# Kernel optimization log

Measured on AMD Instinct MI355X. Metric: run time of the kernel, lower is better.

The kernel has to match this reference:

```python
import jax, jax.numpy as jnp
import numpy as np

LSTM_DIMS = 1024
T = 4096
D = 1024  # per-direction input width; must equal LSTM_DIMS (see original w shape)
CELL_CLIP = 3.0   # tf.raw_ops.BlockLSTM default
FORGET_BIAS = 1.0  # tf.raw_ops.BlockLSTM default


def setup_inputs() -> dict:
    key = jax.random.key(0)
    k1, k2, k3 = jax.random.split(key, 3)
    res_for_1 = jax.random.normal(k1, (1, T, D), dtype=jnp.float32)
    res_back_1 = jax.random.normal(k2, (1, T, D), dtype=jnp.float32)
    # GlorotUniform for w: shape [D + 2*H, 4*H]
    fan_in, fan_out = D + 2 * LSTM_DIMS, 4 * LSTM_DIMS
    limit = np.sqrt(6.0 / (fan_in + fan_out)).astype(np.float32)
    w = jax.random.uniform(k3, (fan_in, fan_out), dtype=jnp.float32,
                           minval=-limit, maxval=limit)
    return {"res_for_1": res_for_1, "res_back_1": res_back_1, "w": w}


def _bilstm(res_for_1, res_back_1, w):
    H = w.shape[1] // 4
    x_dim = 2 * res_for_1.shape[-1]
    # concatenate_lstm: vec[i] = concat(for[i], back[T-1-i]) -> [T, 2D]
    vec_for = jnp.concatenate([res_for_1[0], res_back_1[0][::-1]], axis=-1)
    vec_back = vec_for[::-1]
    xs = jnp.stack([vec_for, vec_back])            # [2, T, 2D]
    w_x, w_h = w[:x_dim], w[x_dim:]                # [2D,4H], [H,4H]
    # precompute input projection as one big GEMM (bias is zeros)
    zx = jnp.einsum('dtf,fg->dtg', xs, w_x)        # [2, T, 4H]

    def step(carry, zx_t):
        c, h = carry
        z = zx_t + h @ w_h                         # [4H]
        zi, zc, zf, zo = jnp.split(z, 4)           # BlockLSTM icfo order
        i = jax.nn.sigmoid(zi)
        ci = jnp.tanh(zc)
        f = jax.nn.sigmoid(zf + FORGET_BIAS)
        cs = jnp.clip(f * c + i * ci, -CELL_CLIP, CELL_CLIP)
        o = jax.nn.sigmoid(zo)
        h = o * jnp.tanh(cs)
        return (cs, h), h

    init = (jnp.zeros((H,), zx.dtype), jnp.zeros((H,), zx.dtype))

    def run(zx_dir):
        _, hs = jax.lax.scan(step, init, zx_dir)
        return hs                                  # [T, H]

    hs = jax.vmap(run)(zx)                         # [2, T, H]
    return hs[0], hs[1]                            # res_for_2, res_back_2


def reference(res_for_1, res_back_1, w):
    return _bilstm(res_for_1, res_back_1, w)
```

## Files before the change

kernel.cpp:

```cpp
#include <hip/hip_runtime.h>

#define T_STEPS 4096
#define HDIM 1024

typedef __bf16 bf16x8 __attribute__((ext_vector_type(8)));
typedef float f32x4 __attribute__((ext_vector_type(4)));
typedef _Float16 half2_t __attribute__((ext_vector_type(2)));

__device__ __forceinline__ unsigned short f2bf(float x) {
  unsigned u = __builtin_bit_cast(unsigned, x);
  u += 0x7fffu + ((u >> 16) & 1u);
  return (unsigned short)(u >> 16);
}
__device__ __forceinline__ float bf2f(unsigned short b) {
  unsigned u = ((unsigned)b) << 16;
  return __builtin_bit_cast(float, u);
}

__global__ __launch_bounds__(256) void build_xs(
    const float* __restrict__ rf, const float* __restrict__ rb,
    unsigned short* __restrict__ xs) {
  int idx = blockIdx.x * 256 + threadIdx.x;
  int e = idx * 4;
  int f = e & 2047;
  int td = e >> 11;
  int t = td & 4095;
  int d = td >> 12;
  bool lower = f < 1024;
  int f2 = f & 1023;
  int trow;
  if (d == 0) trow = lower ? t : (4095 - t);
  else        trow = lower ? (4095 - t) : t;
  const float* src = (lower ? rf : rb) + trow * 1024 + f2;
  float4 v = *(const float4*)src;
  ushort4 o = make_ushort4(f2bf(v.x), f2bf(v.y), f2bf(v.z), f2bf(v.w));
  *(ushort4*)(xs + e) = o;
}

__global__ __launch_bounds__(256) void transpose_wx(
    const float* __restrict__ w, unsigned short* __restrict__ wxT) {
  __shared__ float tile[64][65];
  int bid = blockIdx.x;
  int bf_ = bid / 64;
  int bg = bid % 64;
  int f0 = bf_ * 64, g0 = bg * 64;
  int tid = threadIdx.x;
#pragma unroll
  for (int s = 0; s < 16; ++s) {
    int idx = s * 256 + tid;
    int fl = idx >> 6, gl = idx & 63;
    tile[fl][gl] = w[(size_t)(f0 + fl) * 4096 + g0 + gl];
  }
  __syncthreads();
#pragma unroll
  for (int s = 0; s < 16; ++s) {
    int idx = s * 256 + tid;
    int gl = idx >> 6, fl = idx & 63;
    wxT[(size_t)(g0 + gl) * 2048 + f0 + fl] = f2bf(tile[fl][gl]);
  }
}

__global__ __launch_bounds__(256) void gemm_zx(
    const unsigned short* __restrict__ xs, const unsigned short* __restrict__ wxT,
    unsigned short* __restrict__ zxo) {
  __shared__ uint4 lds[1024];
  char* ldsb = (char*)lds;
  int bid = blockIdx.x;
  int by = bid >> 5;
  int bx = bid & 31;
  int tid = threadIdx.x, lane = tid & 63, wid = tid >> 6;
  int wr = wid >> 1, wc = wid & 1;
  const int arow0 = by * 128, bcol0 = bx * 128;

  f32x4 acc[4][4] = {};

  for (int kt = 0; kt < 64; ++kt) {
    int k0 = kt * 32;
#pragma unroll
    for (int s = 0; s < 2; ++s) {
      int c = tid + 256 * s;
      int L = c * 16;
      int P = L ^ (((L >> 6) & 7) << 4);
      int row = c >> 2, ko = (c & 3) * 8;
      uint4 av = *(const uint4*)(xs  + (size_t)(arow0 + row) * 2048 + k0 + ko);
      uint4 bv = *(const uint4*)(wxT + (size_t)(bcol0 + row) * 2048 + k0 + ko);
      *(uint4*)(ldsb + P) = av;
      *(uint4*)(ldsb + 8192 + P) = bv;
    }
    __syncthreads();

    bf16x8 afr[4], bfr[4];
#pragma unroll
    for (int i = 0; i < 4; ++i) {
      int arow = wr * 64 + i * 16 + (lane & 15);
      int L = arow * 64 + (lane >> 4) * 16;
      int P = L ^ ((arow & 7) << 4);
      afr[i] = *(bf16x8*)(ldsb + P);
      int brow = wc * 64 + i * 16 + (lane & 15);
      int L2 = brow * 64 + (lane >> 4) * 16;
      int P2 = L2 ^ ((brow & 7) << 4);
      bfr[i] = *(bf16x8*)(ldsb + 8192 + P2);
    }
#pragma unroll
    for (int mi = 0; mi < 4; ++mi)
#pragma unroll
      for (int ni = 0; ni < 4; ++ni)
        acc[mi][ni] = __builtin_amdgcn_mfma_f32_16x16x32_bf16(
            afr[mi], bfr[ni], acc[mi][ni], 0, 0, 0);
    __syncthreads();
  }

#pragma unroll
  for (int mi = 0; mi < 4; ++mi)
#pragma unroll
    for (int ni = 0; ni < 4; ++ni)
#pragma unroll
      for (int r = 0; r < 4; ++r) {
        int rrow = arow0 + wr * 64 + mi * 16 + (lane >> 4) * 4 + r;
        int col  = bcol0 + wc * 64 + ni * 16 + (lane & 15);
        zxo[(size_t)rrow * 4096 + col] = f2bf(acc[mi][ni][r]);
      }
}

__global__ __launch_bounds__(256) void pack_whp(
    const float* __restrict__ w, unsigned* __restrict__ whp) {
  int idx = blockIdx.x * 256 + threadIdx.x;
  int gc = idx & 4095;
  int k2 = idx >> 12;
  float w0 = w[(size_t)(2048 + 2 * k2) * 4096 + gc];
  float w1 = w[(size_t)(2048 + 2 * k2 + 1) * 4096 + gc];
  unsigned short a = __builtin_bit_cast(unsigned short, (_Float16)w0);
  unsigned short b = __builtin_bit_cast(unsigned short, (_Float16)w1);
  whp[idx] = ((unsigned)b << 16) | (unsigned)a;
}

__global__ __launch_bounds__(256) void clear_hcom(uint4* __restrict__ p) {
  p[(size_t)blockIdx.x * 256 + threadIdx.x] = uint4{0, 0, 0, 0};
}

__device__ __forceinline__ float sigm(float x) {
  return 1.0f / (1.0f + __expf(-x));
}
__device__ __forceinline__ float tanh_fast(float x) {
  float e = __expf(-2.0f * x);
  return (1.0f - e) / (1.0f + e);
}

__global__ __launch_bounds__(1024, 4) void lstm_rec(
    const unsigned short* __restrict__ zx,
    const unsigned* __restrict__ whp,
    float* __restrict__ hout,
    unsigned* __restrict__ hcom) {
  __shared__ unsigned short hstg[16][64];
  __shared__ float part[2][16][64];

  int bid = blockIdx.x;
  int dir = bid >> 6;
  int bslot = bid & 63;
  int jbase = bslot << 4;
  int tid = threadIdx.x;
  int wave = tid >> 6;
  int lane = tid & 63;
  int jj = lane & 15, g = lane >> 4;
  int gcol = (g << 10) + jbase + jj;

  unsigned wpk[32];
  {
    const unsigned* wp = whp + (size_t)(wave * 32) * 4096 + gcol;
#pragma unroll
    for (int i = 0; i < 32; ++i) wpk[i] = wp[(size_t)i * 4096];
#pragma unroll
    for (int i = 0; i < 32; ++i)
      asm volatile("v_mov_b32 %0, %0" : "+v"(wpk[i]));
  }

  float c_reg = 0.0f;
  const unsigned short* zrow = zx + (size_t)dir * T_STEPS * 4096;
  float* hrow = hout + (size_t)dir * T_STEPS * HDIM;
  unsigned* hcd = hcom + (size_t)dir * T_STEPS * HDIM;
  const unsigned* hp_slice = hcd + wave * 64 + lane;

  for (int t = 0; t < T_STEPS; ++t) {
    float zxv = 0.0f;
    if (wave == 15) zxv = bf2f(zrow[(size_t)t * 4096 + gcol]);

    unsigned short hbits = 0;
    if (t > 0) {
      const unsigned* hp = hp_slice + (size_t)(t - 1) * HDIM;
      unsigned want = (unsigned)t << 16;
      unsigned v;
      do {
        v = __hip_atomic_load(hp, __ATOMIC_RELAXED, __HIP_MEMORY_SCOPE_AGENT);
      } while (v < want);
      hbits = (unsigned short)v;
    }
    hstg[wave][lane] = hbits;
    asm volatile("s_waitcnt lgkmcnt(0)" ::: "memory");

    const unsigned* h2 = (const unsigned*)(&hstg[wave][0]);
    float acc = 0.0f;
#pragma unroll
    for (int i = 0; i < 32; ++i) {
      half2_t hh = __builtin_bit_cast(half2_t, h2[i]);
      half2_t ww = __builtin_bit_cast(half2_t, wpk[i]);
      acc = __builtin_amdgcn_fdot2(ww, hh, acc, false);
    }
    if (wave == 15) acc += zxv;
    part[t & 1][wave][lane] = acc;
    __syncthreads();

    if (wave == 0) {
      float z = 0.f;
#pragma unroll
      for (int q = 0; q < 16; ++q) z += part[t & 1][q][lane];
      float gz = (g == 2) ? z + 1.0f : z;
      float nl = (g == 1) ? tanh_fast(z) : sigm(gz);
      float iv = __shfl(nl, jj, 64);
      float cv = __shfl(nl, 16 + jj, 64);
      float fv = __shfl(nl, 32 + jj, 64);
      float ov = __shfl(nl, 48 + jj, 64);
      if (lane < 16) {
        float cs = fmaf(fv, c_reg, iv * cv);
        cs = fminf(3.0f, fmaxf(-3.0f, cs));
        c_reg = cs;
        float h = ov * tanh_fast(cs);
        if (t + 1 < T_STEPS) {
          unsigned short hb = __builtin_bit_cast(unsigned short, (_Float16)h);
          unsigned pk = ((unsigned)(t + 1) << 16) | (unsigned)hb;
          __hip_atomic_store(&hcd[(size_t)t * HDIM + jbase + lane], pk,
                             __ATOMIC_RELAXED, __HIP_MEMORY_SCOPE_AGENT);
        }
        hrow[(size_t)t * HDIM + jbase + lane] = h;
      }
    }
  }
}

extern "C" void kernel_launch(void* const* d_in, const int* in_sizes, int n_in,
                              void* d_out, int out_size, void* d_ws, size_t ws_size,
                              hipStream_t stream) {
  const float* rf = (const float*)d_in[0];
  const float* rb = (const float*)d_in[1];
  const float* w  = (const float*)d_in[2];
  float* out = (float*)d_out;

  char* ws = (char*)d_ws;
  unsigned short* zx  = (unsigned short*)ws;
  unsigned short* xs  = (unsigned short*)(ws + (64u << 20));
  unsigned*      hcom = (unsigned*)(ws + (64u << 20));
  unsigned short* wxT = (unsigned short*)(ws + (96u << 20));
  unsigned*      whp  = (unsigned*)(ws + (96u << 20));

  build_xs<<<16384, 256, 0, stream>>>(rf, rb, xs);
  transpose_wx<<<2048, 256, 0, stream>>>(w, wxT);
  gemm_zx<<<2048, 256, 0, stream>>>(xs, wxT, zx);
  pack_whp<<<8192, 256, 0, stream>>>(w, whp);
  clear_hcom<<<8192, 256, 0, stream>>>((uint4*)hcom);
  lstm_rec<<<128, 1024, 0, stream>>>(zx, whp, out, hcom);
}
```

Measured before the change: 6.339 ms.

## Pipeline spin-wait loads in asm and defer fp32 output writes to unpack kernel

The single-load atomic spin on the previous step's h value becomes an inline-asm loop that keeps four uncached global loads in flight, cutting the latency of each poll. The per-step fp32 h store in the recurrent loop is dropped, and a separate unpack_out kernel converts the packed fp16 h values from the communication buffer into the output afterward. The output now carries fp16 precision, and the hand-written asm with vcc/exec branching is fragile.

```diff
diff --git a/kernel.cpp b/kernel.cpp
--- a/kernel.cpp
+++ b/kernel.cpp
@@ -149,7 +149,6 @@
 __global__ __launch_bounds__(1024, 4) void lstm_rec(
     const unsigned short* __restrict__ zx,
     const unsigned* __restrict__ whp,
-    float* __restrict__ hout,
     unsigned* __restrict__ hcom) {
   __shared__ unsigned short hstg[16][64];
   __shared__ float part[2][16][64];
@@ -176,7 +175,6 @@
 
   float c_reg = 0.0f;
   const unsigned short* zrow = zx + (size_t)dir * T_STEPS * 4096;
-  float* hrow = hout + (size_t)dir * T_STEPS * HDIM;
   unsigned* hcd = hcom + (size_t)dir * T_STEPS * HDIM;
   const unsigned* hp_slice = hcd + wave * 64 + lane;
 
@@ -186,13 +184,50 @@
 
     unsigned short hbits = 0;
     if (t > 0) {
-      const unsigned* hp = hp_slice + (size_t)(t - 1) * HDIM;
+      unsigned long long a = (unsigned long long)(hp_slice + (size_t)(t - 1) * HDIM);
       unsigned want = (unsigned)t << 16;
-      unsigned v;
-      do {
-        v = __hip_atomic_load(hp, __ATOMIC_RELAXED, __HIP_MEMORY_SCOPE_AGENT);
-      } while (v < want);
-      hbits = (unsigned short)v;
+      unsigned got, p0, p1, p2, p3;
+      asm volatile(
+        "v_mov_b32 %0, 0\n\t"
+        "global_load_dword %2, %6, off sc0 sc1\n\t"
+        "global_load_dword %3, %6, off sc0 sc1\n\t"
+        "global_load_dword %4, %6, off sc0 sc1\n\t"
+        "global_load_dword %5, %6, off sc0 sc1\n\t"
+        "1:\n\t"
+        "s_waitcnt vmcnt(3)\n\t"
+        "v_cmp_le_u32 vcc, %7, %2\n\t"
+        "v_cndmask_b32 %0, %0, %2, vcc\n\t"
+        "global_load_dword %2, %6, off sc0 sc1\n\t"
+        "v_cmp_le_u32 vcc, %7, %0\n\t"
+        "s_andn2_b64 vcc, exec, vcc\n\t"
+        "s_cbranch_scc0 2f\n\t"
+        "s_waitcnt vmcnt(3)\n\t"
+        "v_cmp_le_u32 vcc, %7, %3\n\t"
+        "v_cndmask_b32 %0, %0, %3, vcc\n\t"
+        "global_load_dword %3, %6, off sc0 sc1\n\t"
+        "v_cmp_le_u32 vcc, %7, %0\n\t"
+        "s_andn2_b64 vcc, exec, vcc\n\t"
+        "s_cbranch_scc0 2f\n\t"
+        "s_waitcnt vmcnt(3)\n\t"
+        "v_cmp_le_u32 vcc, %7, %4\n\t"
+        "v_cndmask_b32 %0, %0, %4, vcc\n\t"
+        "global_load_dword %4, %6, off sc0 sc1\n\t"
+        "v_cmp_le_u32 vcc, %7, %0\n\t"
+        "s_andn2_b64 vcc, exec, vcc\n\t"
+        "s_cbranch_scc0 2f\n\t"
+        "s_waitcnt vmcnt(3)\n\t"
+        "v_cmp_le_u32 vcc, %7, %5\n\t"
+        "v_cndmask_b32 %0, %0, %5, vcc\n\t"
+        "global_load_dword %5, %6, off sc0 sc1\n\t"
+        "v_cmp_le_u32 vcc, %7, %0\n\t"
+        "s_andn2_b64 vcc, exec, vcc\n\t"
+        "s_cbranch_scc1 1b\n\t"
+        "2:\n\t"
+        "s_waitcnt vmcnt(0)"
+        : "=&v"(got), "+v"(a), "=&v"(p0), "=&v"(p1), "=&v"(p2), "=&v"(p3)
+        : "v"(a), "v"(want)
+        : "vcc", "memory");
+      hbits = (unsigned short)got;
     }
     hstg[wave][lane] = hbits;
     asm volatile("s_waitcnt lgkmcnt(0)" ::: "memory");
@@ -224,16 +259,25 @@
         cs = fminf(3.0f, fmaxf(-3.0f, cs));
         c_reg = cs;
         float h = ov * tanh_fast(cs);
-        if (t + 1 < T_STEPS) {
-          unsigned short hb = __builtin_bit_cast(unsigned short, (_Float16)h);
-          unsigned pk = ((unsigned)(t + 1) << 16) | (unsigned)hb;
-          __hip_atomic_store(&hcd[(size_t)t * HDIM + jbase + lane], pk,
-                             __ATOMIC_RELAXED, __HIP_MEMORY_SCOPE_AGENT);
-        }
-        hrow[(size_t)t * HDIM + jbase + lane] = h;
+        unsigned short hb = __builtin_bit_cast(unsigned short, (_Float16)h);
+        unsigned pk = ((unsigned)(t + 1) << 16) | (unsigned)hb;
+        __hip_atomic_store(&hcd[(size_t)t * HDIM + jbase + lane], pk,
+                           __ATOMIC_RELAXED, __HIP_MEMORY_SCOPE_AGENT);
       }
     }
   }
+}
+
+__global__ __launch_bounds__(256) void unpack_out(
+    const unsigned* __restrict__ hcom, float* __restrict__ out) {
+  int i = blockIdx.x * 256 + threadIdx.x;
+  uint4 v = ((const uint4*)hcom)[i];
+  float4 o;
+  o.x = (float)__builtin_bit_cast(_Float16, (unsigned short)v.x);
+  o.y = (float)__builtin_bit_cast(_Float16, (unsigned short)v.y);
+  o.z = (float)__builtin_bit_cast(_Float16, (unsigned short)v.z);
+  o.w = (float)__builtin_bit_cast(_Float16, (unsigned short)v.w);
+  ((float4*)out)[i] = o;
 }
 
 extern "C" void kernel_launch(void* const* d_in, const int* in_sizes, int n_in,
@@ -256,5 +300,6 @@
   gemm_zx<<<2048, 256, 0, stream>>>(xs, wxT, zx);
   pack_whp<<<8192, 256, 0, stream>>>(w, whp);
   clear_hcom<<<8192, 256, 0, stream>>>((uint4*)hcom);
-  lstm_rec<<<128, 1024, 0, stream>>>(zx, whp, out, hcom);
-}
+  lstm_rec<<<128, 1024, 0, stream>>>(zx, whp, hcom);
+  unpack_out<<<8192, 256, 0, stream>>>(hcom, out);
+}
```

New measurement: 7.421 ms. +17.1%, slower.

## Drop fp32 output store from recurrence; unpack fp16 h buffer afterward

Applied to the files above, without the earlier changes.

The recurrent kernel no longer writes fp32 h to the output each step. It writes only the packed fp16 h with a step tag to the communication buffer, and a new kernel converts that buffer to fp32 output after the recurrence. The LDS read of h is widened to 128-bit loads, and the dot product is split across four accumulators to shorten the dependency chain. This takes a global store off the serial critical path, but the output now carries fp16 precision and costs an extra pass over memory.

```diff
diff --git a/kernel.cpp b/kernel.cpp
--- a/kernel.cpp
+++ b/kernel.cpp
@@ -149,7 +149,6 @@
 __global__ __launch_bounds__(1024, 4) void lstm_rec(
     const unsigned short* __restrict__ zx,
     const unsigned* __restrict__ whp,
-    float* __restrict__ hout,
     unsigned* __restrict__ hcom) {
   __shared__ unsigned short hstg[16][64];
   __shared__ float part[2][16][64];
@@ -176,7 +175,6 @@
 
   float c_reg = 0.0f;
   const unsigned short* zrow = zx + (size_t)dir * T_STEPS * 4096;
-  float* hrow = hout + (size_t)dir * T_STEPS * HDIM;
   unsigned* hcd = hcom + (size_t)dir * T_STEPS * HDIM;
   const unsigned* hp_slice = hcd + wave * 64 + lane;
 
@@ -197,14 +195,21 @@
     hstg[wave][lane] = hbits;
     asm volatile("s_waitcnt lgkmcnt(0)" ::: "memory");
 
-    const unsigned* h2 = (const unsigned*)(&hstg[wave][0]);
-    float acc = 0.0f;
-#pragma unroll
-    for (int i = 0; i < 32; ++i) {
-      half2_t hh = __builtin_bit_cast(half2_t, h2[i]);
-      half2_t ww = __builtin_bit_cast(half2_t, wpk[i]);
-      acc = __builtin_amdgcn_fdot2(ww, hh, acc, false);
-    }
+    const uint4* h4p = (const uint4*)(&hstg[wave][0]);
+    float ac0 = 0.f, ac1 = 0.f, ac2 = 0.f, ac3 = 0.f;
+#pragma unroll
+    for (int i = 0; i < 8; ++i) {
+      uint4 hv = h4p[i];
+      ac0 = __builtin_amdgcn_fdot2(__builtin_bit_cast(half2_t, wpk[4 * i + 0]),
+                                   __builtin_bit_cast(half2_t, hv.x), ac0, false);
+      ac1 = __builtin_amdgcn_fdot2(__builtin_bit_cast(half2_t, wpk[4 * i + 1]),
+                                   __builtin_bit_cast(half2_t, hv.y), ac1, false);
+      ac2 = __builtin_amdgcn_fdot2(__builtin_bit_cast(half2_t, wpk[4 * i + 2]),
+                                   __builtin_bit_cast(half2_t, hv.z), ac2, false);
+      ac3 = __builtin_amdgcn_fdot2(__builtin_bit_cast(half2_t, wpk[4 * i + 3]),
+                                   __builtin_bit_cast(half2_t, hv.w), ac3, false);
+    }
+    float acc = (ac0 + ac1) + (ac2 + ac3);
     if (wave == 15) acc += zxv;
     part[t & 1][wave][lane] = acc;
     __syncthreads();
@@ -224,16 +229,25 @@
         cs = fminf(3.0f, fmaxf(-3.0f, cs));
         c_reg = cs;
         float h = ov * tanh_fast(cs);
-        if (t + 1 < T_STEPS) {
-          unsigned short hb = __builtin_bit_cast(unsigned short, (_Float16)h);
-          unsigned pk = ((unsigned)(t + 1) << 16) | (unsigned)hb;
-          __hip_atomic_store(&hcd[(size_t)t * HDIM + jbase + lane], pk,
-                             __ATOMIC_RELAXED, __HIP_MEMORY_SCOPE_AGENT);
-        }
-        hrow[(size_t)t * HDIM + jbase + lane] = h;
+        unsigned short hb = __builtin_bit_cast(unsigned short, (_Float16)h);
+        unsigned pk = ((unsigned)(t + 1) << 16) | (unsigned)hb;
+        __hip_atomic_store(&hcd[(size_t)t * HDIM + jbase + lane], pk,
+                           __ATOMIC_RELAXED, __HIP_MEMORY_SCOPE_AGENT);
       }
     }
   }
+}
+
+__global__ __launch_bounds__(256) void unpack_out(
+    const unsigned* __restrict__ hcom, float* __restrict__ out) {
+  int i = blockIdx.x * 256 + threadIdx.x;
+  uint4 v = ((const uint4*)hcom)[i];
+  float4 o;
+  o.x = (float)__builtin_bit_cast(_Float16, (unsigned short)v.x);
+  o.y = (float)__builtin_bit_cast(_Float16, (unsigned short)v.y);
+  o.z = (float)__builtin_bit_cast(_Float16, (unsigned short)v.z);
+  o.w = (float)__builtin_bit_cast(_Float16, (unsigned short)v.w);
+  ((float4*)out)[i] = o;
 }
 
 extern "C" void kernel_launch(void* const* d_in, const int* in_sizes, int n_in,
@@ -256,5 +270,6 @@
   gemm_zx<<<2048, 256, 0, stream>>>(xs, wxT, zx);
   pack_whp<<<8192, 256, 0, stream>>>(w, whp);
   clear_hcom<<<8192, 256, 0, stream>>>((uint4*)hcom);
-  lstm_rec<<<128, 1024, 0, stream>>>(zx, whp, out, hcom);
-}
+  lstm_rec<<<128, 1024, 0, stream>>>(zx, whp, hcom);
+  unpack_out<<<8192, 256, 0, stream>>>(hcom, out);
+}
```

After: 6.348 ms (median of 2 runs). No clear change (+0.1%).
